# Kernel tuning notes

Hardware: AMD Instinct MI355X
Metric: run time of the kernel (lower is better)

The kernel has to match this reference:

```python
import jax, jax.numpy as jnp
import numpy as np

N_EMBED = 1024
N_HEADS = 16
HEAD_SIZE = N_EMBED // N_HEADS
B, T = 4, 2048
LN_EPS = 1e-5


def _layer_norm(x, gamma, beta):
    mu = jnp.mean(x, axis=-1, keepdims=True)
    var = jnp.var(x, axis=-1, keepdims=True)
    return (x - mu) * jax.lax.rsqrt(var + LN_EPS) * gamma + beta


def setup_inputs() -> dict:
    key = jax.random.key(0)
    ks = jax.random.split(key, 12)
    s = 1.0 / np.sqrt(N_EMBED)
    sh = 1.0 / np.sqrt(4 * N_EMBED)
    return {
        "x": jax.random.normal(ks[0], (B, T, N_EMBED), jnp.float32),
        "Wk": jax.random.uniform(ks[1], (N_EMBED, N_EMBED), jnp.float32, -s, s),
        "Wq": jax.random.uniform(ks[2], (N_EMBED, N_EMBED), jnp.float32, -s, s),
        "Wv": jax.random.uniform(ks[3], (N_EMBED, N_EMBED), jnp.float32, -s, s),
        "Wproj": jax.random.uniform(ks[4], (N_EMBED, N_EMBED), jnp.float32, -s, s),
        "bproj": jax.random.uniform(ks[5], (N_EMBED,), jnp.float32, -s, s),
        "W1": jax.random.uniform(ks[6], (N_EMBED, 4 * N_EMBED), jnp.float32, -s, s),
        "b1": jax.random.uniform(ks[7], (4 * N_EMBED,), jnp.float32, -s, s),
        "W2": jax.random.uniform(ks[8], (4 * N_EMBED, N_EMBED), jnp.float32, -sh, sh),
        "b2": jax.random.uniform(ks[9], (N_EMBED,), jnp.float32, -sh, sh),
        "g1": jnp.ones((N_EMBED,), jnp.float32),
        "beta1": jnp.zeros((N_EMBED,), jnp.float32),
        "g2": jnp.ones((N_EMBED,), jnp.float32),
        "beta2": jnp.zeros((N_EMBED,), jnp.float32),
    }


def reference(x, Wk, Wq, Wv, Wproj, bproj, W1, b1, W2, b2, g1, beta1, g2, beta2):
    Bt, Tt, C = x.shape
    h = _layer_norm(x, g1, beta1)
    # project and split heads: (B, H, T, D)
    def heads(W):
        return (h @ W).reshape(Bt, Tt, N_HEADS, HEAD_SIZE).transpose(0, 2, 1, 3)
    q, k, v = heads(Wq), heads(Wk), heads(Wv)
    wei = jnp.einsum("bhtd,bhsd->bhts", q, k) / np.sqrt(HEAD_SIZE)
    causal = jnp.tril(jnp.ones((Tt, Tt), bool))
    wei = jnp.where(causal, wei, -jnp.inf)
    wei = jax.nn.softmax(wei, axis=-1)
    out = jnp.einsum("bhts,bhsd->bhtd", wei, v)
    out = out.transpose(0, 2, 1, 3).reshape(Bt, Tt, C)
    x = x + out @ Wproj + bproj
    h2 = _layer_norm(x, g2, beta2)
    ff = jax.nn.relu(h2 @ W1 + b1) @ W2 + b2
    return x + ff
```

## Files before the change

### kernel.cpp

```cpp
#include <hip/hip_runtime.h>
#include <stdint.h>

typedef __bf16 bf16x8 __attribute__((ext_vector_type(8)));
typedef float f32x4 __attribute__((ext_vector_type(4)));
typedef unsigned short u16x8 __attribute__((ext_vector_type(8)));
typedef unsigned short u16x4 __attribute__((ext_vector_type(4)));
typedef unsigned int u32x2 __attribute__((ext_vector_type(2)));
typedef float fvec4 __attribute__((ext_vector_type(4)));

__device__ __forceinline__ unsigned short f2b(float f) {
  unsigned u = __builtin_bit_cast(unsigned, f);
  return (unsigned short)((u + 0x7fffu + ((u >> 16) & 1u)) >> 16);
}

__device__ __forceinline__ bf16x8 ldfrag(const unsigned short* p) {
  return __builtin_bit_cast(bf16x8, *(const u16x8*)p);
}

__device__ __forceinline__ float fexp2(float x) {
  float r;
  asm("v_exp_f32 %0, %1" : "=v"(r) : "v"(x));
  return r;
}

__device__ __forceinline__ unsigned cvtpk(float a, float b) {
  unsigned r;
  asm("v_cvt_pk_bf16_f32 %0, %1, %2" : "=v"(r) : "v"(a), "v"(b));
  return r;
}

__device__ __forceinline__ void gload_lds16(const void* g, void* l) {
  auto gp = reinterpret_cast<const __attribute__((address_space(1))) void*>(
      reinterpret_cast<uintptr_t>(g));
  auto lp = reinterpret_cast<__attribute__((address_space(3))) void*>(
      reinterpret_cast<uintptr_t>(l));
  __builtin_amdgcn_global_load_lds(gp, lp, 16, 0, 0);
}

__global__ void transpose_cast(const float* __restrict__ W, unsigned short* __restrict__ Wt,
                               int K, int N) {
  __shared__ float tile[32][33];
  const int n0 = blockIdx.x * 32, k0 = blockIdx.y * 32;
  const int tx = threadIdx.x, ty = threadIdx.y;
#pragma unroll
  for (int j = 0; j < 4; ++j)
    tile[ty + j * 8][tx] = W[(size_t)(k0 + ty + j * 8) * N + n0 + tx];
  __syncthreads();
#pragma unroll
  for (int j = 0; j < 4; ++j)
    Wt[(size_t)(n0 + ty + j * 8) * K + k0 + tx] = f2b(tile[tx][ty + j * 8]);
}

__global__ void ln_kernel(const float* __restrict__ X, const float* __restrict__ g,
                          const float* __restrict__ be, unsigned short* __restrict__ H) {
  const int row = (blockIdx.x * blockDim.x + threadIdx.x) >> 6;
  const int l = threadIdx.x & 63;
  const float* xr = X + (size_t)row * 1024;
  fvec4 v[4];
  float s = 0.f, sq = 0.f;
#pragma unroll
  for (int i = 0; i < 4; ++i) {
    v[i] = *(const fvec4*)(xr + i * 256 + l * 4);
#pragma unroll
    for (int j = 0; j < 4; ++j) { s += v[i][j]; sq += v[i][j] * v[i][j]; }
  }
#pragma unroll
  for (int off = 32; off >= 1; off >>= 1) {
    s += __shfl_xor(s, off);
    sq += __shfl_xor(sq, off);
  }
  const float mean = s * (1.f / 1024.f);
  const float var = sq * (1.f / 1024.f) - mean * mean;
  const float rstd = rsqrtf(var + 1e-5f);
#pragma unroll
  for (int i = 0; i < 4; ++i) {
    const int col = i * 256 + l * 4;
    fvec4 gg = *(const fvec4*)(g + col);
    fvec4 bb = *(const fvec4*)(be + col);
    u16x4 o;
#pragma unroll
    for (int j = 0; j < 4; ++j) o[j] = f2b((v[i][j] - mean) * rstd * gg[j] + bb[j]);
    *(u16x4*)(H + (size_t)row * 1024 + col) = o;
  }
}

template <int EPI>
__global__ __launch_bounds__(512, 1) void gemmS(
    const unsigned short* __restrict__ A, const unsigned short* __restrict__ Bt,
    const float* __restrict__ bias, const float* __restrict__ resid,
    float* __restrict__ Cf, unsigned short* __restrict__ Cb,
    unsigned short* __restrict__ pK, unsigned short* __restrict__ pVT,
    int N, int K, int ntiles) {
  constexpr int ASZ = 16384;
  constexpr int BSZ = 32768;
  constexpr int BUFSZ = ASZ + BSZ;
  __shared__ __align__(16) char lds[3 * BUFSZ];

  const int tid = threadIdx.x;
  const int w = tid >> 6, l = tid & 63;
  const int wr = w >> 2, wc = w & 3;
  const int kg = l >> 4, fr = l & 15;
  const int nblk = (int)gridDim.x;

  int Aoff[2][4], Boff[2][4];
#pragma unroll
  for (int kk = 0; kk < 2; ++kk) {
#pragma unroll
    for (int m = 0; m < 4; ++m) {
      const int r = wr * 64 + m * 16 + fr;
      Aoff[kk][m] = r * 128 + (((kk * 4 + kg) ^ (r & 7)) << 4);
    }
#pragma unroll
    for (int n = 0; n < 4; ++n) {
      const int rn = wc * 64 + n * 16 + fr;
      Boff[kk][n] = ASZ + rn * 128 + (((kk * 4 + kg) ^ (rn & 7)) << 4);
    }
  }

  for (int tl = (int)blockIdx.x; tl < ntiles; tl += nblk) {
    if (tl != (int)blockIdx.x) {
      asm volatile("s_waitcnt vmcnt(0) lgkmcnt(0)" ::: "memory");
      __builtin_amdgcn_s_barrier();
    }
    const int round = tl >> 8;
    const int i = tl & 255;
    const int xcd = i & 7;
    const int s = i >> 3;
    const size_t am0 = (size_t)(xcd * 8 + (s >> 2)) * 128;
    const size_t bn0 = (size_t)(round * 4 + (s & 3)) * 256;

    const char* src[6];
#pragma unroll
    for (int u = 0; u < 2; ++u) {
      const int flat = u * 512 + tid;
      const int row = flat >> 3, c = flat & 7;
      src[u] = (const char*)(A + (am0 + row) * K) + ((c ^ (row & 7)) << 4);
    }
#pragma unroll
    for (int u = 0; u < 4; ++u) {
      const int flat = u * 512 + tid;
      const int row = flat >> 3, c = flat & 7;
      src[2 + u] = (const char*)(Bt + (bn0 + row) * K) + ((c ^ (row & 7)) << 4);
    }

    f32x4 acc[4][4];
#pragma unroll
    for (int m = 0; m < 4; ++m)
#pragma unroll
      for (int n = 0; n < 4; ++n) acc[m][n] = (f32x4){0.f, 0.f, 0.f, 0.f};

    auto stage_a = [&](int sb) {
      char* Ld = lds + sb * BUFSZ;
      gload_lds16(src[0], Ld + tid * 16);
      src[0] += 128;
      gload_lds16(src[1], Ld + 8192 + tid * 16);
      src[1] += 128;
    };
    auto stage_b = [&](int sb) {
      char* Ld = lds + sb * BUFSZ;
      gload_lds16(src[2], Ld + ASZ + tid * 16);
      src[2] += 128;
      gload_lds16(src[3], Ld + ASZ + 8192 + tid * 16);
      src[3] += 128;
    };
    auto stage_c = [&](int sb) {
      char* Ld = lds + sb * BUFSZ;
      gload_lds16(src[4], Ld + ASZ + 16384 + tid * 16);
      src[4] += 128;
      gload_lds16(src[5], Ld + ASZ + 24576 + tid * 16);
      src[5] += 128;
    };

    const int NT = K >> 6;
    stage_a(0);
    stage_b(0);
    stage_c(0);
    stage_a(1);
    stage_b(1);
    stage_c(1);
    asm volatile("s_waitcnt vmcnt(6)" ::: "memory");
    __builtin_amdgcn_s_barrier();

    int cb0 = 0, sb = 2;
    for (int kt = 0; kt < NT; ++kt) {
      const bool pre = (kt + 2 < NT);
      if (pre) stage_a(sb);
      {
        bf16x8 af[4], bf[4];
#pragma unroll
        for (int m = 0; m < 4; ++m)
          af[m] = ldfrag((const unsigned short*)(lds + cb0 + Aoff[0][m]));
#pragma unroll
        for (int n = 0; n < 4; ++n)
          bf[n] = ldfrag((const unsigned short*)(lds + cb0 + Boff[0][n]));
        if (pre) stage_b(sb);
        __builtin_amdgcn_s_setprio(1);
#pragma unroll
        for (int m = 0; m < 4; ++m)
#pragma unroll
          for (int n = 0; n < 4; ++n)
            acc[m][n] = __builtin_amdgcn_mfma_f32_16x16x32_bf16(af[m], bf[n], acc[m][n], 0, 0, 0);
        __builtin_amdgcn_s_setprio(0);
      }
      {
        bf16x8 af[4], bf[4];
#pragma unroll
        for (int m = 0; m < 4; ++m)
          af[m] = ldfrag((const unsigned short*)(lds + cb0 + Aoff[1][m]));
#pragma unroll
        for (int n = 0; n < 4; ++n)
          bf[n] = ldfrag((const unsigned short*)(lds + cb0 + Boff[1][n]));
        if (pre) stage_c(sb);
        __builtin_amdgcn_s_setprio(1);
#pragma unroll
        for (int m = 0; m < 4; ++m)
#pragma unroll
          for (int n = 0; n < 4; ++n)
            acc[m][n] = __builtin_amdgcn_mfma_f32_16x16x32_bf16(af[m], bf[n], acc[m][n], 0, 0, 0);
        __builtin_amdgcn_s_setprio(0);
      }
      if (pre) {
        asm volatile("s_waitcnt vmcnt(6)" ::: "memory");
        __builtin_amdgcn_s_barrier();
      } else if (kt + 1 < NT) {
        asm volatile("s_waitcnt vmcnt(0)" ::: "memory");
        __builtin_amdgcn_s_barrier();
      }
      cb0 += BUFSZ;
      if (cb0 == 3 * BUFSZ) cb0 = 0;
      sb += 1;
      if (sb == 3) sb = 0;
    }

#pragma unroll
    for (int m = 0; m < 4; ++m) {
      const size_t row0 = am0 + wr * 64 + m * 16 + kg * 4;
#pragma unroll
      for (int n = 0; n < 4; ++n) {
        const size_t col = bn0 + wc * 64 + n * 16 + fr;
        if (EPI == 3) {
          if (bn0 < 1024) {
#pragma unroll
            for (int r = 0; r < 4; ++r) Cb[(row0 + r) * 1024 + col] = f2b(acc[m][n][r]);
          } else if (bn0 < 2048) {
#pragma unroll
            for (int r = 0; r < 4; ++r) pK[(row0 + r) * 1024 + col - 1024] = f2b(acc[m][n][r]);
          } else {
            const int c2 = (int)col - 2048;
            const int hh = c2 >> 6, dd = c2 & 63;
            const int bb = (int)(row0 >> 11), tt = (int)(row0 & 2047);
            u16x4 pv;
#pragma unroll
            for (int r = 0; r < 4; ++r) pv[r] = f2b(acc[m][n][r]);
            *(u16x4*)(pVT + (((size_t)bb * 16 + hh) * 64 + dd) * 2048 + tt) = pv;
          }
        } else {
          const float bv = (EPI >= 1) ? bias[col] : 0.f;
#pragma unroll
          for (int r = 0; r < 4; ++r) {
            const size_t idx = (row0 + r) * N + col;
            float v = acc[m][n][r] + bv;
            if (EPI == 1) v = fmaxf(v, 0.f);
            if (EPI == 2) {
              Cf[idx] = v + resid[idx];
            } else {
              Cb[idx] = f2b(v);
            }
          }
        }
      }
    }
  }
}

#define PSTR 72
#define SC2 0.18033688f
__global__ __launch_bounds__(256, 2) void attn_kernel(const unsigned short* __restrict__ Qb,
                                                      const unsigned short* __restrict__ Kb,
                                                      const unsigned short* __restrict__ VT,
                                                      unsigned short* __restrict__ ATT) {
  __shared__ __align__(16) char ldsK[3 * 8192];
  __shared__ __align__(16) unsigned short Pl[4][64 * PSTR];
  const int tid = threadIdx.x;
  const int w = tid >> 6, l = tid & 63;
  const int kg = l >> 4, fr = l & 15;
  const int bh = blockIdx.x;
  const int b = bh >> 4, h = bh & 15;
  const int yy = (int)blockIdx.y;
  const int qt = (yy < 4) ? 7 - yy : yy - 4;
  const int q0 = qt * 256 + w * 64;
  const size_t rbase = (size_t)b * 2048;
  const unsigned short* vtb = VT + (size_t)bh * 64 * 2048;
  const f32x4 fz = {0.f, 0.f, 0.f, 0.f};

  const int rowoff = tid >> 3;
  const int cbsw = ((tid & 7) * 16) ^ ((rowoff & 7) << 4);
  const char* ksrc = (const char*)(Kb + rbase * 1024 + h * 64) + (size_t)rowoff * 2048 + cbsw;

  int koff[4][2];
#pragma unroll
  for (int sg = 0; sg < 4; ++sg)
#pragma unroll
    for (int c = 0; c < 2; ++c)
      koff[sg][c] = (sg * 16 + fr) * 128 + ((c * 64 + kg * 16) ^ ((fr & 7) << 4));

  bf16x8 bq[4][2];
#pragma unroll
  for (int qg = 0; qg < 4; ++qg) {
    const unsigned short* qrow = Qb + (rbase + q0 + qg * 16 + fr) * 1024 + h * 64;
#pragma unroll
    for (int c = 0; c < 2; ++c) bq[qg][c] = ldfrag(qrow + c * 32 + kg * 8);
  }

  f32x4 o[4][4];
#pragma unroll
  for (int qg = 0; qg < 4; ++qg)
#pragma unroll
    for (int nd = 0; nd < 4; ++nd) o[qg][nd] = (f32x4){0.f, 0.f, 0.f, 0.f};
  float m_run2[4] = {-1e30f, -1e30f, -1e30f, -1e30f};
  float l_run[4] = {0.f, 0.f, 0.f, 0.f};

  auto stage = [&](int t, int sbuf) {
    gload_lds16(ksrc + (size_t)(t * 64) * 2048, ldsK + sbuf * 8192 + tid * 16);
    gload_lds16(ksrc + (size_t)(t * 64 + 32) * 2048, ldsK + sbuf * 8192 + 4096 + tid * 16);
  };

  auto softmax_qg = [&](int qg, int s0, f32x4 (&stq)[4]) -> float {
    const int qa = q0 + qg * 16 + fr;
    float vals[16];
    if (s0 + 63 <= q0 + qg * 16) {
#pragma unroll
      for (int sg = 0; sg < 4; ++sg)
#pragma unroll
        for (int r = 0; r < 4; ++r) vals[sg * 4 + r] = stq[sg][r];
    } else {
#pragma unroll
      for (int sg = 0; sg < 4; ++sg)
#pragma unroll
        for (int r = 0; r < 4; ++r) {
          const int sa = s0 + sg * 16 + kg * 4 + r;
          vals[sg * 4 + r] = (sa > qa) ? -1e30f : stq[sg][r];
        }
    }
    float m5[5];
#pragma unroll
    for (int i = 0; i < 5; ++i)
      m5[i] = fmaxf(fmaxf(vals[3 * i], vals[3 * i + 1]), vals[3 * i + 2]);
    const float vmax =
        fmaxf(fmaxf(fmaxf(m5[0], m5[1]), m5[2]), fmaxf(fmaxf(m5[3], m5[4]), vals[15]));
    const float tm2 = vmax * SC2;
    if (__any(tm2 > m_run2[qg] + 8.f)) {
      float tmax2 = tm2;
      tmax2 = fmaxf(tmax2, __shfl_xor(tmax2, 16));
      tmax2 = fmaxf(tmax2, __shfl_xor(tmax2, 32));
      const float m_new2 = fmaxf(m_run2[qg], tmax2);
      const float alpha = fexp2(m_run2[qg] - m_new2);
      m_run2[qg] = m_new2;
      l_run[qg] *= alpha;
      float al[4];
#pragma unroll
      for (int r = 0; r < 4; ++r) al[r] = __shfl(alpha, kg * 4 + r);
#pragma unroll
      for (int nd = 0; nd < 4; ++nd)
#pragma unroll
        for (int r = 0; r < 4; ++r) o[qg][nd][r] *= al[r];
    }
    const float nm2 = -m_run2[qg];
    float psum = 0.f;
    unsigned pk[8];
#pragma unroll
    for (int i = 0; i < 8; ++i) {
      const float p0 = fexp2(__builtin_fmaf(vals[2 * i], SC2, nm2));
      const float p1 = fexp2(__builtin_fmaf(vals[2 * i + 1], SC2, nm2));
      psum += p0 + p1;
      pk[i] = cvtpk(p0, p1);
    }
#pragma unroll
    for (int sg = 0; sg < 4; ++sg) {
      u32x2 w2 = {pk[2 * sg], pk[2 * sg + 1]};
      *(u32x2*)(&Pl[w][(qg * 16 + fr) * PSTR + sg * 16 + kg * 4]) = w2;
    }
    return psum;
  };

  auto compute = [&](int s0, int cbb) {
    if (s0 > q0 + 63) return;
    bf16x8 vb[4][2];
#pragma unroll
    for (int nd = 0; nd < 4; ++nd)
#pragma unroll
      for (int ks = 0; ks < 2; ++ks)
        vb[nd][ks] = ldfrag(vtb + (size_t)(nd * 16 + fr) * 2048 + s0 + ks * 32 + kg * 8);

    float psv[4];
#pragma unroll
    for (int qp = 0; qp < 2; ++qp) {
      f32x4 st[4][2];
#pragma unroll
      for (int sg = 0; sg < 4; ++sg) {
        const bf16x8 ka0 = ldfrag((const unsigned short*)(ldsK + cbb + koff[sg][0]));
        const bf16x8 ka1 = ldfrag((const unsigned short*)(ldsK + cbb + koff[sg][1]));
#pragma unroll
        for (int qh = 0; qh < 2; ++qh)
          st[sg][qh] = __builtin_amdgcn_mfma_f32_16x16x32_bf16(
              ka1, bq[qp * 2 + qh][1],
              __builtin_amdgcn_mfma_f32_16x16x32_bf16(ka0, bq[qp * 2 + qh][0], fz, 0, 0, 0),
              0, 0, 0);
      }
#pragma unroll
      for (int qh = 0; qh < 2; ++qh) {
        f32x4 stq[4];
#pragma unroll
        for (int sg = 0; sg < 4; ++sg) stq[sg] = st[sg][qh];
        psv[qp * 2 + qh] = softmax_qg(qp * 2 + qh, s0, stq);
      }
    }

    {
      float a[4], c[4];
#pragma unroll
      for (int qg = 0; qg < 4; ++qg) a[qg] = __shfl_xor(psv[qg], 16);
#pragma unroll
      for (int qg = 0; qg < 4; ++qg) psv[qg] += a[qg];
#pragma unroll
      for (int qg = 0; qg < 4; ++qg) c[qg] = __shfl_xor(psv[qg], 32);
#pragma unroll
      for (int qg = 0; qg < 4; ++qg) l_run[qg] += psv[qg] + c[qg];
    }

#pragma unroll
    for (int qg = 0; qg < 4; ++qg)
#pragma unroll
      for (int ks = 0; ks < 2; ++ks) {
        const bf16x8 pa = ldfrag(&Pl[w][(qg * 16 + fr) * PSTR + ks * 32 + kg * 8]);
#pragma unroll
        for (int nd = 0; nd < 4; ++nd)
          o[qg][nd] = __builtin_amdgcn_mfma_f32_16x16x32_bf16(pa, vb[nd][ks], o[qg][nd], 0, 0, 0);
      }
  };

  const int NT = 4 * qt + 4;
  stage(0, 0);
  stage(1, 1);
  asm volatile("s_waitcnt vmcnt(2)" ::: "memory");
  __builtin_amdgcn_s_barrier();
  int cb = 0, sb = 2;
  for (int t = 0; t < NT; ++t) {
    if (t + 2 < NT) stage(t + 2, sb);
    compute(t * 64, cb * 8192);
    if (t + 2 < NT) {
      asm volatile("s_waitcnt vmcnt(2)" ::: "memory");
      __builtin_amdgcn_s_barrier();
    } else if (t + 1 < NT) {
      asm volatile("s_waitcnt vmcnt(0)" ::: "memory");
      __builtin_amdgcn_s_barrier();
    }
    cb += 1; if (cb == 3) cb = 0;
    sb += 1; if (sb == 3) sb = 0;
  }

#pragma unroll
  for (int qg = 0; qg < 4; ++qg) {
    const float li = __builtin_amdgcn_rcpf(l_run[qg]);
    float linv[4];
#pragma unroll
    for (int r = 0; r < 4; ++r) linv[r] = __shfl(li, kg * 4 + r);
#pragma unroll
    for (int nd = 0; nd < 4; ++nd)
#pragma unroll
      for (int r = 0; r < 4; ++r) {
        const size_t row = rbase + q0 + qg * 16 + kg * 4 + r;
        ATT[row * 1024 + h * 64 + nd * 16 + fr] = f2b(o[qg][nd][r] * linv[r]);
      }
  }
}

extern "C" void kernel_launch(void* const* d_in, const int* in_sizes, int n_in, void* d_out,
                              int out_size, void* d_ws, size_t ws_size, hipStream_t stream) {
  const float* x = (const float*)d_in[0];
  const float* Wk = (const float*)d_in[1];
  const float* Wq = (const float*)d_in[2];
  const float* Wv = (const float*)d_in[3];
  const float* Wproj = (const float*)d_in[4];
  const float* bproj = (const float*)d_in[5];
  const float* W1 = (const float*)d_in[6];
  const float* b1 = (const float*)d_in[7];
  const float* W2 = (const float*)d_in[8];
  const float* b2 = (const float*)d_in[9];
  const float* g1 = (const float*)d_in[10];
  const float* beta1 = (const float*)d_in[11];
  const float* g2 = (const float*)d_in[12];
  const float* beta2 = (const float*)d_in[13];
  float* out = (float*)d_out;
  unsigned short* wsu = (unsigned short*)d_ws;

  const size_t o_qkvW = 0;
  const size_t o_projW = o_qkvW + 3072 * 1024;
  const size_t o_W1 = o_projW + 1024 * 1024;
  const size_t o_W2 = o_W1 + 4096 * 1024;
  const size_t o_H = o_W2 + 1024 * 4096;
  const size_t o_Q = o_H + (size_t)8192 * 1024;
  const size_t o_K = o_Q + (size_t)8192 * 1024;
  const size_t o_VT = o_K + (size_t)8192 * 1024;
  const size_t o_ATT = o_VT + (size_t)8192 * 1024;
  const size_t o_FF1 = o_Q;

  dim3 tpb(32, 8);
  transpose_cast<<<dim3(32, 32), tpb, 0, stream>>>(Wq, wsu + o_qkvW, 1024, 1024);
  transpose_cast<<<dim3(32, 32), tpb, 0, stream>>>(Wk, wsu + o_qkvW + 1024 * 1024, 1024, 1024);
  transpose_cast<<<dim3(32, 32), tpb, 0, stream>>>(Wv, wsu + o_qkvW + 2 * 1024 * 1024, 1024, 1024);
  transpose_cast<<<dim3(32, 32), tpb, 0, stream>>>(Wproj, wsu + o_projW, 1024, 1024);
  transpose_cast<<<dim3(128, 32), tpb, 0, stream>>>(W1, wsu + o_W1, 1024, 4096);
  transpose_cast<<<dim3(32, 128), tpb, 0, stream>>>(W2, wsu + o_W2, 4096, 1024);

  ln_kernel<<<2048, 256, 0, stream>>>(x, g1, beta1, wsu + o_H);

  gemmS<3><<<256, 512, 0, stream>>>(wsu + o_H, wsu + o_qkvW, nullptr, nullptr, nullptr,
                                    wsu + o_Q, wsu + o_K, wsu + o_VT, 3072, 1024, 768);

  attn_kernel<<<dim3(64, 8), 256, 0, stream>>>(wsu + o_Q, wsu + o_K, wsu + o_VT, wsu + o_ATT);

  gemmS<2><<<256, 512, 0, stream>>>(wsu + o_ATT, wsu + o_projW, bproj, x, out, nullptr,
                                    nullptr, nullptr, 1024, 1024, 256);

  ln_kernel<<<2048, 256, 0, stream>>>(out, g2, beta2, wsu + o_H);

  gemmS<1><<<256, 512, 0, stream>>>(wsu + o_H, wsu + o_W1, b1, nullptr, nullptr,
                                    wsu + o_FF1, nullptr, nullptr, 4096, 1024, 1024);

  gemmS<2><<<256, 512, 0, stream>>>(wsu + o_FF1, wsu + o_W2, b2, out, out, nullptr,
                                    nullptr, nullptr, 1024, 4096, 256);
}
```

Baseline: 329.8 us.

## Split attention block into 8 waves of 32 query rows each

The attention kernel now runs 512 threads per block, with each of 8 wavefronts handling 32 query rows instead of 4 waves handling 64. K-tile staging is spread over all 512 threads with a single load each, and the wait counts are adjusted to match. The aim is more waves per CU to hide latency and cut per-wave register pressure. In exchange, each wave reloads the V fragments from global memory for half as many queries, which doubles redundant V traffic.

```diff
diff --git a/kernel.cpp b/kernel.cpp
--- a/kernel.cpp
+++ b/kernel.cpp
@@ -275,12 +275,12 @@
 
 #define PSTR 72
 #define SC2 0.18033688f
-__global__ __launch_bounds__(256, 2) void attn_kernel(const unsigned short* __restrict__ Qb,
+__global__ __launch_bounds__(512, 4) void attn_kernel(const unsigned short* __restrict__ Qb,
                                                       const unsigned short* __restrict__ Kb,
                                                       const unsigned short* __restrict__ VT,
                                                       unsigned short* __restrict__ ATT) {
   __shared__ __align__(16) char ldsK[3 * 8192];
-  __shared__ __align__(16) unsigned short Pl[4][64 * PSTR];
+  __shared__ __align__(16) unsigned short Pl[8][32 * PSTR];
   const int tid = threadIdx.x;
   const int w = tid >> 6, l = tid & 63;
   const int kg = l >> 4, fr = l & 15;
@@ -288,7 +288,7 @@
   const int b = bh >> 4, h = bh & 15;
   const int yy = (int)blockIdx.y;
   const int qt = (yy < 4) ? 7 - yy : yy - 4;
-  const int q0 = qt * 256 + w * 64;
+  const int q0 = qt * 256 + w * 32;
   const size_t rbase = (size_t)b * 2048;
   const unsigned short* vtb = VT + (size_t)bh * 64 * 2048;
   const f32x4 fz = {0.f, 0.f, 0.f, 0.f};
@@ -304,25 +304,24 @@
     for (int c = 0; c < 2; ++c)
       koff[sg][c] = (sg * 16 + fr) * 128 + ((c * 64 + kg * 16) ^ ((fr & 7) << 4));
 
-  bf16x8 bq[4][2];
-#pragma unroll
-  for (int qg = 0; qg < 4; ++qg) {
+  bf16x8 bq[2][2];
+#pragma unroll
+  for (int qg = 0; qg < 2; ++qg) {
     const unsigned short* qrow = Qb + (rbase + q0 + qg * 16 + fr) * 1024 + h * 64;
 #pragma unroll
     for (int c = 0; c < 2; ++c) bq[qg][c] = ldfrag(qrow + c * 32 + kg * 8);
   }
 
-  f32x4 o[4][4];
-#pragma unroll
-  for (int qg = 0; qg < 4; ++qg)
+  f32x4 o[2][4];
+#pragma unroll
+  for (int qg = 0; qg < 2; ++qg)
 #pragma unroll
     for (int nd = 0; nd < 4; ++nd) o[qg][nd] = (f32x4){0.f, 0.f, 0.f, 0.f};
-  float m_run2[4] = {-1e30f, -1e30f, -1e30f, -1e30f};
-  float l_run[4] = {0.f, 0.f, 0.f, 0.f};
+  float m_run2[2] = {-1e30f, -1e30f};
+  float l_run[2] = {0.f, 0.f};
 
   auto stage = [&](int t, int sbuf) {
     gload_lds16(ksrc + (size_t)(t * 64) * 2048, ldsK + sbuf * 8192 + tid * 16);
-    gload_lds16(ksrc + (size_t)(t * 64 + 32) * 2048, ldsK + sbuf * 8192 + 4096 + tid * 16);
   };
 
   auto softmax_qg = [&](int qg, int s0, f32x4 (&stq)[4]) -> float {
@@ -384,7 +383,7 @@
   };
 
   auto compute = [&](int s0, int cbb) {
-    if (s0 > q0 + 63) return;
+    if (s0 > q0 + 31) return;
     bf16x8 vb[4][2];
 #pragma unroll
     for (int nd = 0; nd < 4; ++nd)
@@ -392,44 +391,40 @@
       for (int ks = 0; ks < 2; ++ks)
         vb[nd][ks] = ldfrag(vtb + (size_t)(nd * 16 + fr) * 2048 + s0 + ks * 32 + kg * 8);
 
-    float psv[4];
-#pragma unroll
-    for (int qp = 0; qp < 2; ++qp) {
-      f32x4 st[4][2];
-#pragma unroll
-      for (int sg = 0; sg < 4; ++sg) {
-        const bf16x8 ka0 = ldfrag((const unsigned short*)(ldsK + cbb + koff[sg][0]));
-        const bf16x8 ka1 = ldfrag((const unsigned short*)(ldsK + cbb + koff[sg][1]));
-#pragma unroll
-        for (int qh = 0; qh < 2; ++qh)
-          st[sg][qh] = __builtin_amdgcn_mfma_f32_16x16x32_bf16(
-              ka1, bq[qp * 2 + qh][1],
-              __builtin_amdgcn_mfma_f32_16x16x32_bf16(ka0, bq[qp * 2 + qh][0], fz, 0, 0, 0),
-              0, 0, 0);
-      }
-#pragma unroll
-      for (int qh = 0; qh < 2; ++qh) {
-        f32x4 stq[4];
-#pragma unroll
-        for (int sg = 0; sg < 4; ++sg) stq[sg] = st[sg][qh];
-        psv[qp * 2 + qh] = softmax_qg(qp * 2 + qh, s0, stq);
-      }
+    f32x4 st[4][2];
+#pragma unroll
+    for (int sg = 0; sg < 4; ++sg) {
+      const bf16x8 ka0 = ldfrag((const unsigned short*)(ldsK + cbb + koff[sg][0]));
+      const bf16x8 ka1 = ldfrag((const unsigned short*)(ldsK + cbb + koff[sg][1]));
+#pragma unroll
+      for (int qh = 0; qh < 2; ++qh)
+        st[sg][qh] = __builtin_amdgcn_mfma_f32_16x16x32_bf16(
+            ka1, bq[qh][1],
+            __builtin_amdgcn_mfma_f32_16x16x32_bf16(ka0, bq[qh][0], fz, 0, 0, 0), 0, 0, 0);
+    }
+
+    float psv[2];
+#pragma unroll
+    for (int qh = 0; qh < 2; ++qh) {
+      f32x4 stq[4];
+#pragma unroll
+      for (int sg = 0; sg < 4; ++sg) stq[sg] = st[sg][qh];
+      psv[qh] = softmax_qg(qh, s0, stq);
     }
 
     {
-      float a[4], c[4];
-#pragma unroll
-      for (int qg = 0; qg < 4; ++qg) a[qg] = __shfl_xor(psv[qg], 16);
-#pragma unroll
-      for (int qg = 0; qg < 4; ++qg) psv[qg] += a[qg];
-#pragma unroll
-      for (int qg = 0; qg < 4; ++qg) c[qg] = __shfl_xor(psv[qg], 32);
-#pragma unroll
-      for (int qg = 0; qg < 4; ++qg) l_run[qg] += psv[qg] + c[qg];
-    }
-
-#pragma unroll
-    for (int qg = 0; qg < 4; ++qg)
+      const float a0 = __shfl_xor(psv[0], 16);
+      const float a1 = __shfl_xor(psv[1], 16);
+      psv[0] += a0;
+      psv[1] += a1;
+      const float b0 = __shfl_xor(psv[0], 32);
+      const float b1 = __shfl_xor(psv[1], 32);
+      l_run[0] += psv[0] + b0;
+      l_run[1] += psv[1] + b1;
+    }
+
+#pragma unroll
+    for (int qg = 0; qg < 2; ++qg)
 #pragma unroll
       for (int ks = 0; ks < 2; ++ks) {
         const bf16x8 pa = ldfrag(&Pl[w][(qg * 16 + fr) * PSTR + ks * 32 + kg * 8]);
@@ -442,14 +437,14 @@
   const int NT = 4 * qt + 4;
   stage(0, 0);
   stage(1, 1);
-  asm volatile("s_waitcnt vmcnt(2)" ::: "memory");
+  asm volatile("s_waitcnt vmcnt(1)" ::: "memory");
   __builtin_amdgcn_s_barrier();
   int cb = 0, sb = 2;
   for (int t = 0; t < NT; ++t) {
     if (t + 2 < NT) stage(t + 2, sb);
     compute(t * 64, cb * 8192);
     if (t + 2 < NT) {
-      asm volatile("s_waitcnt vmcnt(2)" ::: "memory");
+      asm volatile("s_waitcnt vmcnt(1)" ::: "memory");
       __builtin_amdgcn_s_barrier();
     } else if (t + 1 < NT) {
       asm volatile("s_waitcnt vmcnt(0)" ::: "memory");
@@ -460,7 +455,7 @@
   }
 
 #pragma unroll
-  for (int qg = 0; qg < 4; ++qg) {
+  for (int qg = 0; qg < 2; ++qg) {
     const float li = __builtin_amdgcn_rcpf(l_run[qg]);
     float linv[4];
 #pragma unroll
@@ -518,7 +513,7 @@
   gemmS<3><<<256, 512, 0, stream>>>(wsu + o_H, wsu + o_qkvW, nullptr, nullptr, nullptr,
                                     wsu + o_Q, wsu + o_K, wsu + o_VT, 3072, 1024, 768);
 
-  attn_kernel<<<dim3(64, 8), 256, 0, stream>>>(wsu + o_Q, wsu + o_K, wsu + o_VT, wsu + o_ATT);
+  attn_kernel<<<dim3(64, 8), 512, 0, stream>>>(wsu + o_Q, wsu + o_K, wsu + o_VT, wsu + o_ATT);
 
   gemmS<2><<<256, 512, 0, stream>>>(wsu + o_ATT, wsu + o_projW, bproj, x, out, nullptr,
                                     nullptr, nullptr, 1024, 1024, 256);
```

New measurement: 442.6 us. 1.34x slower.
